# Performance work log

Hardware: AMD Instinct MI355X
Metric: run time of the kernel (lower is better)

Reference implementation:

```python
import jax, jax.numpy as jnp
import numpy as np

DIM = 256; DIM_HEAD = 32; HEADS = DIM // DIM_HEAD; WSZ = 8; D4 = DIM // 4
EPS = 1e-5
SCALE = DIM_HEAD ** -0.5


def _rel_pos_indices(wsz):
    pos = np.arange(wsz)
    grid = np.stack(np.meshgrid(pos, pos, indexing='ij')).reshape(2, -1).T  # (w*w, 2)
    rel = grid[:, None] - grid[None, :] + wsz - 1
    return jnp.asarray((rel * np.array([2 * wsz - 1, 1])).sum(-1))  # (w*w, w*w)


def _ln(x, g, b):
    m = x.mean(-1, keepdims=True)
    v = jnp.var(x, axis=-1, keepdims=True)
    return (x - m) / jnp.sqrt(v + EPS) * g + b


def setup_inputs() -> dict:
    key = jax.random.key(0)
    ks = jax.random.split(key, 8)
    inner = HEADS * DIM_HEAD
    def n(k, shape, s=0.02):
        return jax.random.normal(k, shape, dtype=jnp.float32) * s
    return {
        "x": jax.random.normal(ks[0], (2, DIM, 256, 256), dtype=jnp.float32),
        "norm_g": jnp.ones((1, DIM, 1, 1), jnp.float32),
        "norm_b": jnp.zeros((1, DIM, 1, 1), jnp.float32),
        "w_qkv": n(ks[1], (3 * inner, DIM)),
        "w_out": n(ks[2], (DIM, inner)),
        "b_out": jnp.zeros((DIM,), jnp.float32),
        "dpb_w1": n(ks[3], (D4, 2), 0.5), "dpb_b1": jnp.zeros((D4,), jnp.float32),
        "dpb_g1": jnp.ones((D4,), jnp.float32), "dpb_beta1": jnp.zeros((D4,), jnp.float32),
        "dpb_w2": n(ks[4], (D4, D4), 0.1), "dpb_b2": jnp.zeros((D4,), jnp.float32),
        "dpb_g2": jnp.ones((D4,), jnp.float32), "dpb_beta2": jnp.zeros((D4,), jnp.float32),
        "dpb_w3": n(ks[5], (D4, D4), 0.1), "dpb_b3": jnp.zeros((D4,), jnp.float32),
        "dpb_g3": jnp.ones((D4,), jnp.float32), "dpb_beta3": jnp.zeros((D4,), jnp.float32),
        "dpb_w4": n(ks[6], (1, D4), 0.1), "dpb_b4": jnp.zeros((1,), jnp.float32),
    }


def reference(x, norm_g, norm_b, w_qkv, w_out, b_out,
              dpb_w1, dpb_b1, dpb_g1, dpb_beta1,
              dpb_w2, dpb_b2, dpb_g2, dpb_beta2,
              dpb_w3, dpb_b3, dpb_g3, dpb_beta3,
              dpb_w4, dpb_b4):
    B, D, H, W = x.shape
    nh, nw = H // WSZ, W // WSZ
    # channel-first LayerNorm (stats over dim=1, biased variance)
    mean = x.mean(axis=1, keepdims=True)
    var = jnp.var(x, axis=1, keepdims=True)
    xn = (x - mean) / jnp.sqrt(var + EPS) * norm_g + norm_b
    # 'short' windowing: b d (h s1) (w s2) -> (b h w) d (s1 s2)
    xw = xn.reshape(B, D, nh, WSZ, nw, WSZ).transpose(0, 2, 4, 1, 3, 5)
    xw = xw.reshape(B * nh * nw, D, WSZ * WSZ)
    # 1x1 conv QKV == matmul over channel dim
    qkv = jnp.einsum('ed,bdn->ben', w_qkv, xw)
    q, k, v = jnp.split(qkv, 3, axis=1)
    to_heads = lambda t: t.reshape(-1, HEADS, DIM_HEAD, WSZ * WSZ).transpose(0, 1, 3, 2)
    q, k, v = to_heads(q) * SCALE, to_heads(k), to_heads(v)
    sim = jnp.einsum('bhid,bhjd->bhij', q, k)  # [Bw, H, 64, 64]
    # dynamic position bias MLP over relative coordinates in [-wsz, wsz]
    pos = jnp.arange(-WSZ, WSZ + 1, dtype=x.dtype)
    rel = jnp.stack(jnp.meshgrid(pos, pos, indexing='ij')).reshape(2, -1).T  # ((2w+1)^2, 2)
    h1 = jax.nn.relu(_ln(rel @ dpb_w1.T + dpb_b1, dpb_g1, dpb_beta1))
    h2 = jax.nn.relu(_ln(h1 @ dpb_w2.T + dpb_b2, dpb_g2, dpb_beta2))
    h3 = jax.nn.relu(_ln(h2 @ dpb_w3.T + dpb_b3, dpb_g3, dpb_beta3))
    biases = (h3 @ dpb_w4.T + dpb_b4)[:, 0]
    sim = sim + biases[_rel_pos_indices(WSZ)]
    attn = jax.nn.softmax(sim, axis=-1)
    out = jnp.einsum('bhij,bhjd->bhid', attn, v)
    # b h (x y) d -> b (h d) (x y)
    out = out.transpose(0, 1, 3, 2).reshape(-1, HEADS * DIM_HEAD, WSZ * WSZ)
    out = jnp.einsum('de,ben->bdn', w_out, out) + b_out[None, :, None]
    # (b h w) d s1 s2 -> b d (h s1) (w s2)
    out = out.reshape(B, nh, nw, D, WSZ, WSZ).transpose(0, 3, 1, 4, 2, 5).reshape(B, D, H, W)
    return out
```

## Files before the change

kernel.cpp:

```cpp
#include <hip/hip_runtime.h>


typedef __attribute__((ext_vector_type(8))) short bf16x8;
typedef __attribute__((ext_vector_type(4))) short bf16x4;
typedef __attribute__((ext_vector_type(4))) float f32x4;

#define LOG2E    1.44269504088896f
#define QK_SCALE 0.17677669529663687f

__device__ __forceinline__ short f2b(float f) {
  union { float f; unsigned u; } v; v.f = f;
  unsigned r = v.u + 0x7FFFu + ((v.u >> 16) & 1u);
  return (short)(r >> 16);
}

__device__ __forceinline__ unsigned pk2(float a, float b) {
  union { float f; unsigned u; } ua, ub; ua.f = a; ub.f = b;
#if __has_builtin(__builtin_amdgcn_perm)
  return __builtin_amdgcn_perm(ub.u + 0x8000u, ua.u + 0x8000u, 0x07060302u);
#else
  return ((ua.u + 0x8000u) >> 16) | ((ub.u + 0x8000u) & 0xFFFF0000u);
#endif
}

__device__ __forceinline__ bf16x8 mk8(unsigned a, unsigned b, unsigned c, unsigned d) {
  union { unsigned u[4]; bf16x8 v; } x; x.u[0] = a; x.u[1] = b; x.u[2] = c; x.u[3] = d;
  return x.v;
}
__device__ __forceinline__ bf16x4 mk4(unsigned a, unsigned b) {
  union { unsigned u[2]; bf16x4 v; } x; x.u[0] = a; x.u[1] = b; return x.v;
}

__device__ __forceinline__ f32x4 mfma16(bf16x4 a, bf16x4 b, f32x4 c) {
#if __has_builtin(__builtin_amdgcn_mfma_f32_16x16x16bf16_1k)
  return __builtin_amdgcn_mfma_f32_16x16x16bf16_1k(a, b, c, 0, 0, 0);
#else
  f32x4 d;
  asm volatile("v_mfma_f32_16x16x16_bf16 %0, %1, %2, %3"
               : "=&v"(d) : "v"(a), "v"(b), "v"(c));
  return d;
#endif
}

__global__ __launch_bounds__(256)
void wconv_kernel(const float* __restrict__ wqkv, const float* __restrict__ wout,
                  short* __restrict__ wq_t, short* __restrict__ wo_t) {
  int t = (blockIdx.x * 256 + threadIdx.x) * 8;
  if (t < 196608) {
    int blk = t >> 9, l = (t & 511) >> 3;
    int et = blk >> 3, kt = blk & 7;
    int e = et * 16 + (l & 15);
    int d = kt * 32 + (l >> 4) * 8;
    const float* src = wqkv + e * 256 + d;
    float sc = (e < 256) ? QK_SCALE * LOG2E : 1.0f;
    bf16x8 pk;
    #pragma unroll
    for (int el = 0; el < 8; ++el) pk[el] = f2b(src[el] * sc);
    *(bf16x8*)(wq_t + t) = pk;
  } else if (t < 262144) {
    int o = t - 196608;
    int blk = o >> 9, l = (o & 511) >> 3;
    int dt = blk >> 3, kt = blk & 7;
    int dout = dt * 16 + (l & 15);
    int e = kt * 32 + (l >> 4) * 8;
    const float* src = wout + dout * 256 + e;
    bf16x8 pk;
    #pragma unroll
    for (int el = 0; el < 8; ++el) pk[el] = f2b(src[el]);
    *(bf16x8*)(wo_t + o) = pk;
  }
}

__device__ __forceinline__ float wave_sum64(float v) {
  v += __shfl_xor(v, 1);  v += __shfl_xor(v, 2);  v += __shfl_xor(v, 4);
  v += __shfl_xor(v, 8);  v += __shfl_xor(v, 16); v += __shfl_xor(v, 32);
  return v;
}

__global__ __launch_bounds__(64)
void dpb_kernel(const float* __restrict__ w1, const float* __restrict__ b1,
                const float* __restrict__ g1, const float* __restrict__ be1,
                const float* __restrict__ w2, const float* __restrict__ b2,
                const float* __restrict__ g2, const float* __restrict__ be2,
                const float* __restrict__ w3, const float* __restrict__ b3,
                const float* __restrict__ g3, const float* __restrict__ be3,
                const float* __restrict__ w4, const float* __restrict__ b4,
                float* __restrict__ sb) {
  __shared__ float h[64];
  __shared__ float wbuf[4096];
  const int f = threadIdx.x;
  const int pos = blockIdx.x;
  const float py = (float)(pos / 17) - 8.0f;
  const float px = (float)(pos % 17) - 8.0f;

  float a = py * w1[2 * f] + px * w1[2 * f + 1] + b1[f];
  {
    float m = wave_sum64(a) * (1.f / 64.f);
    float d = a - m;
    float var = wave_sum64(d * d) * (1.f / 64.f);
    a = fmaxf(d * rsqrtf(var + 1e-5f) * g1[f] + be1[f], 0.f);
  }
  h[f] = a;
  __threadfence_block();

  #pragma unroll 8
  for (int k = 0; k < 64; ++k) wbuf[k * 64 + f] = w2[k * 64 + f];
  __threadfence_block();
  float acc = b2[f];
  #pragma unroll 8
  for (int k = 0; k < 64; ++k) {
    int g = (k + f) & 63;
    acc += wbuf[f * 64 + g] * h[g];
  }
  {
    float m = wave_sum64(acc) * (1.f / 64.f);
    float d = acc - m;
    float var = wave_sum64(d * d) * (1.f / 64.f);
    acc = fmaxf(d * rsqrtf(var + 1e-5f) * g2[f] + be2[f], 0.f);
  }
  __threadfence_block();
  h[f] = acc;
  __threadfence_block();

  #pragma unroll 8
  for (int k = 0; k < 64; ++k) wbuf[k * 64 + f] = w3[k * 64 + f];
  __threadfence_block();
  float acc3 = b3[f];
  #pragma unroll 8
  for (int k = 0; k < 64; ++k) {
    int g = (k + f) & 63;
    acc3 += wbuf[f * 64 + g] * h[g];
  }
  {
    float m = wave_sum64(acc3) * (1.f / 64.f);
    float d = acc3 - m;
    float var = wave_sum64(d * d) * (1.f / 64.f);
    acc3 = fmaxf(d * rsqrtf(var + 1e-5f) * g3[f] + be3[f], 0.f);
  }
  float o = wave_sum64(w4[f] * acc3);
  if (f == 0) sb[pos] = o + b4[0];
}

__global__ __launch_bounds__(512)
void expand_kernel(const float* __restrict__ sb, float* __restrict__ tblf) {
  int idx = blockIdx.x * 512 + threadIdx.x;
  int it = idx >> 10, jt = (idx >> 8) & 3, ln = (idx >> 2) & 63, jj = idx & 3;
  int rr = ln & 15, gg = ln >> 4;
  int i = it * 16 + rr;
  int j = jt * 16 + gg * 4 + jj;
  int dy = (i >> 3) - (j >> 3) + 7;
  int dx = (i & 7) - (j & 7) + 7;
  tblf[idx] = sb[dy * 15 + dx] * LOG2E;
}

#define SM_XA   0
#define SM_PS   65536
#define SM_SIZE 73728
#define XASWZ(p) ((((p) & 7) << 4) ^ ((((p) >> 3) & 3) << 7))

__global__ __launch_bounds__(512)
void attn_kernel(const float* __restrict__ x, const float* __restrict__ gnorm,
                 const float* __restrict__ bnorm, const short* __restrict__ wq_t,
                 const short* __restrict__ wo_t, const float* __restrict__ bout,
                 const float* __restrict__ tblf, float* __restrict__ out) {
  __shared__ __align__(16) char smem[SM_SIZE];
  const int t = threadIdx.x;
  const int lane = t & 63;
  const int w = t >> 6;
  const int r = lane & 15;
  const int gq = lane >> 4;

  const int bid = blockIdx.x;
  const int b   = bid >> 9;
  const int wh  = (bid >> 4) & 31;
  const int ww2 = bid & 15;
  const int R = wh * 8, C = ww2 * 16;

  const int n = lane;
  const int d0 = w * 32;
  float* PS = (float*)(smem + SM_PS);
  float xv[2][32];
  #pragma unroll
  for (int h = 0; h < 2; ++h) {
    const float* xb = x + (((size_t)(b * 256 + d0)) << 16) +
                      (R + 4 * h + (n >> 4)) * 256 + C + (n & 15);
    float s1 = 0.f, s2v = 0.f;
    #pragma unroll
    for (int i = 0; i < 32; ++i) {
      float v = xb[(size_t)i << 16];
      xv[h][i] = v; s1 += v; s2v += v * v;
    }
    PS[h * 1024 + w * 64 + n] = s1;
    PS[h * 1024 + 512 + w * 64 + n] = s2v;
  }
  __syncthreads();
  #pragma unroll
  for (int h = 0; h < 2; ++h) {
    float a = 0.f, q2 = 0.f;
    #pragma unroll
    for (int dg = 0; dg < 8; ++dg) {
      a  += PS[h * 1024 + dg * 64 + n];
      q2 += PS[h * 1024 + 512 + dg * 64 + n];
    }
    float mean = a * (1.f / 256.f);
    float var = q2 * (1.f / 256.f) - mean * mean;
    float rstd = rsqrtf(var + 1e-5f);
    int p2 = (4 * h + (n >> 4)) * 16 + (n & 15);
    #pragma unroll
    for (int c = 0; c < 4; ++c) {
      float xn[8];
      #pragma unroll
      for (int e = 0; e < 8; ++e) {
        int d = d0 + c * 8 + e;
        xn[e] = (xv[h][c * 8 + e] - mean) * rstd * gnorm[d] + bnorm[d];
      }
      *(bf16x8*)(smem + SM_XA + (p2 << 9) + ((((d0 + c * 8) << 1)) ^ XASWZ(p2))) =
          mk8(pk2(xn[0], xn[1]), pk2(xn[2], xn[3]), pk2(xn[4], xn[5]), pk2(xn[6], xn[7]));
    }
  }
  __syncthreads();

  const f32x4 vzero = {0.f, 0.f, 0.f, 0.f};

  #define QKV_SWAP(PP, ACC)                                                     \
    {                                                                           \
      _Pragma("unroll")                                                         \
      for (int nt = 0; nt < 2; ++nt)                                            \
        _Pragma("unroll")                                                       \
        for (int t4 = 0; t4 < 4; ++t4) ACC[nt][t4] = vzero;                     \
      _Pragma("unroll")                                                         \
      for (int kt = 0; kt < 8; ++kt) {                                          \
        bf16x8 bfr0 = *(const bf16x8*)(wq_t + (((((PP) * 16 + w * 2 + 0) * 8 + kt) << 9) + lane * 8)); \
        bf16x8 bfr1 = *(const bf16x8*)(wq_t + (((((PP) * 16 + w * 2 + 1) * 8 + kt) << 9) + lane * 8)); \
        bf16x8 afr[4];                                                          \
        _Pragma("unroll")                                                       \
        for (int t4 = 0; t4 < 4; ++t4) {                                        \
          int p2 = (t4 * 2 + (r >> 3)) * 16 + wl * 8 + (r & 7);                 \
          afr[t4] = *(const bf16x8*)(smem + SM_XA + (p2 << 9) + ((((kt * 32 + gq * 8) << 1)) ^ XASWZ(p2))); \
        }                                                                       \
        _Pragma("unroll")                                                       \
        for (int t4 = 0; t4 < 4; ++t4) {                                        \
          ACC[0][t4] = __builtin_amdgcn_mfma_f32_16x16x32_bf16(bfr0, afr[t4], ACC[0][t4], 0, 0, 0); \
          ACC[1][t4] = __builtin_amdgcn_mfma_f32_16x16x32_bf16(bfr1, afr[t4], ACC[1][t4], 0, 0, 0); \
        }                                                                       \
      }                                                                         \
    }

  f32x4 o2[2][2][4];
  #pragma unroll
  for (int wl = 0; wl < 2; ++wl) {
    bf16x4 kpk[2][4], qpk[2][4];
    {
      f32x4 acc[2][4];
      QKV_SWAP(1, acc);
      #pragma unroll
      for (int kb = 0; kb < 2; ++kb)
        #pragma unroll
        for (int jt = 0; jt < 4; ++jt)
          kpk[kb][jt] = mk4(pk2(acc[kb][jt][0], acc[kb][jt][1]),
                            pk2(acc[kb][jt][2], acc[kb][jt][3]));
    }
    {
      f32x4 acc[2][4];
      QKV_SWAP(0, acc);
      #pragma unroll
      for (int kb = 0; kb < 2; ++kb)
        #pragma unroll
        for (int it = 0; it < 4; ++it)
          qpk[kb][it] = mk4(pk2(acc[kb][it][0], acc[kb][it][1]),
                            pk2(acc[kb][it][2], acc[kb][it][3]));
    }
    bf16x4 va8[4][2];
    {
      f32x4 vacc[4][2];
      #pragma unroll
      for (int mt = 0; mt < 4; ++mt)
        #pragma unroll
        for (int nt = 0; nt < 2; ++nt) vacc[mt][nt] = vzero;
      #pragma unroll
      for (int kt = 0; kt < 8; ++kt) {
        bf16x8 bfr0 = *(const bf16x8*)(wq_t + ((((2 * 16 + w * 2 + 0) * 8 + kt) << 9) + lane * 8));
        bf16x8 bfr1 = *(const bf16x8*)(wq_t + ((((2 * 16 + w * 2 + 1) * 8 + kt) << 9) + lane * 8));
        bf16x8 afr[4];
        #pragma unroll
        for (int mt = 0; mt < 4; ++mt) {
          int p2 = (mt * 2 + (r >> 3)) * 16 + wl * 8 + (r & 7);
          afr[mt] = *(const bf16x8*)(smem + SM_XA + (p2 << 9) + ((((kt * 32 + gq * 8) << 1)) ^ XASWZ(p2)));
        }
        #pragma unroll
        for (int mt = 0; mt < 4; ++mt) {
          vacc[mt][0] = __builtin_amdgcn_mfma_f32_16x16x32_bf16(afr[mt], bfr0, vacc[mt][0], 0, 0, 0);
          vacc[mt][1] = __builtin_amdgcn_mfma_f32_16x16x32_bf16(afr[mt], bfr1, vacc[mt][1], 0, 0, 0);
        }
      }
      #pragma unroll
      for (int mt = 0; mt < 4; ++mt)
        #pragma unroll
        for (int nt = 0; nt < 2; ++nt)
          va8[mt][nt] = mk4(pk2(vacc[mt][nt][0], vacc[mt][nt][1]),
                            pk2(vacc[mt][nt][2], vacc[mt][nt][3]));
    }

    #pragma unroll
    for (int nt = 0; nt < 2; ++nt)
      #pragma unroll
      for (int it = 0; it < 4; ++it) o2[wl][nt][it] = vzero;
    __builtin_amdgcn_s_setprio(1);
    #pragma unroll
    for (int it = 0; it < 4; ++it) {
      f32x4 sc[4];
      #pragma unroll
      for (int jt = 0; jt < 4; ++jt) {
        sc[jt] = mfma16(kpk[0][jt], qpk[0][it], vzero);
        sc[jt] = mfma16(kpk[1][jt], qpk[1][it], sc[jt]);
      }
      float m0 = -1e30f;
      #pragma unroll
      for (int jt = 0; jt < 4; ++jt) {
        f32x4 bj = *(const f32x4*)(tblf + (((it * 4 + jt) * 64 + lane) << 2));
        #pragma unroll
        for (int jj = 0; jj < 4; ++jj) {
          sc[jt][jj] += bj[jj];
          m0 = fmaxf(m0, sc[jt][jj]);
        }
      }
      m0 = fmaxf(m0, __shfl_xor(m0, 16));
      m0 = fmaxf(m0, __shfl_xor(m0, 32));
      float sum = 0.f;
      #pragma unroll
      for (int jt = 0; jt < 4; ++jt)
        #pragma unroll
        for (int jj = 0; jj < 4; ++jj) {
          float e = exp2f(sc[jt][jj] - m0);
          sc[jt][jj] = e; sum += e;
        }
      sum += __shfl_xor(sum, 16);
      sum += __shfl_xor(sum, 32);
      float pinv = 1.0f / sum;
      bf16x4 ppk[4];
      #pragma unroll
      for (int jt = 0; jt < 4; ++jt)
        ppk[jt] = mk4(pk2(sc[jt][0] * pinv, sc[jt][1] * pinv),
                      pk2(sc[jt][2] * pinv, sc[jt][3] * pinv));
      #pragma unroll
      for (int mt = 0; mt < 4; ++mt)
        #pragma unroll
        for (int nt = 0; nt < 2; ++nt)
          o2[wl][nt][it] = mfma16(va8[mt][nt], ppk[mt], o2[wl][nt][it]);
    }
    __builtin_amdgcn_s_setprio(0);
  }
  __syncthreads();

  #pragma unroll
  for (int wl = 0; wl < 2; ++wl)
    #pragma unroll
    for (int nt = 0; nt < 2; ++nt)
      #pragma unroll
      for (int it = 0; it < 4; ++it) {
        int pw = it * 16 + r;
        int p2 = ((pw >> 3) << 4) + (wl << 3) + (pw & 7);
        int e = (w << 5) + (nt << 4) + (gq << 2);
        *(bf16x4*)(smem + SM_XA + (p2 << 9) + (((e << 1)) ^ XASWZ(p2))) =
            mk4(pk2(o2[wl][nt][it][0], o2[wl][nt][it][1]),
                pk2(o2[wl][nt][it][2], o2[wl][nt][it][3]));
      }
  __syncthreads();

  float bov[2];
  bov[0] = bout[w * 32 + r];
  bov[1] = bout[w * 32 + 16 + r];

  #pragma unroll
  for (int ck = 0; ck < 2; ++ck) {
    f32x4 c3[4][2];
    #pragma unroll
    for (int mt = 0; mt < 4; ++mt)
      #pragma unroll
      for (int nt = 0; nt < 2; ++nt) c3[mt][nt] = vzero;
    __builtin_amdgcn_s_setprio(1);
    #pragma unroll
    for (int kt = 0; kt < 8; ++kt) {
      bf16x8 woB[2];
      #pragma unroll
      for (int nt = 0; nt < 2; ++nt)
        woB[nt] = *(const bf16x8*)(wo_t + ((((w * 2 + nt) * 8 + kt) << 9) + lane * 8));
      bf16x8 af[4];
      #pragma unroll
      for (int mt = 0; mt < 4; ++mt) {
        int p2 = ck * 64 + mt * 16 + r;
        af[mt] = *(const bf16x8*)(smem + SM_XA + (p2 << 9) + ((((kt * 32 + gq * 8) << 1)) ^ XASWZ(p2)));
      }
      #pragma unroll
      for (int mt = 0; mt < 4; ++mt)
        #pragma unroll
        for (int nt = 0; nt < 2; ++nt)
          c3[mt][nt] = __builtin_amdgcn_mfma_f32_16x16x32_bf16(af[mt], woB[nt], c3[mt][nt], 0, 0, 0);
    }
    __builtin_amdgcn_s_setprio(0);
    #pragma unroll
    for (int mt = 0; mt < 4; ++mt)
      #pragma unroll
      for (int nt = 0; nt < 2; ++nt) {
        int dout = w * 32 + nt * 16 + r;
        int row = ck * 4 + mt;
        f32x4 v = c3[mt][nt];
        v[0] += bov[nt]; v[1] += bov[nt]; v[2] += bov[nt]; v[3] += bov[nt];
        *(f32x4*)(out + (((size_t)(b * 256 + dout)) << 16) + (R + row) * 256 + C + gq * 4) = v;
      }
  }
  #undef QKV_SWAP
}

extern "C" void kernel_launch(void* const* d_in, const int* in_sizes, int n_in,
                              void* d_out, int out_size, void* d_ws, size_t ws_size,
                              hipStream_t stream) {
  const float* x     = (const float*)d_in[0];
  const float* gnorm = (const float*)d_in[1];
  const float* bnorm = (const float*)d_in[2];
  const float* wqkv  = (const float*)d_in[3];
  const float* wout  = (const float*)d_in[4];
  const float* bout  = (const float*)d_in[5];
  const float* w1  = (const float*)d_in[6];
  const float* b1  = (const float*)d_in[7];
  const float* g1  = (const float*)d_in[8];
  const float* be1 = (const float*)d_in[9];
  const float* w2  = (const float*)d_in[10];
  const float* b2  = (const float*)d_in[11];
  const float* g2  = (const float*)d_in[12];
  const float* be2 = (const float*)d_in[13];
  const float* w3  = (const float*)d_in[14];
  const float* b3  = (const float*)d_in[15];
  const float* g3  = (const float*)d_in[16];
  const float* be3 = (const float*)d_in[17];
  const float* w4  = (const float*)d_in[18];
  const float* b4  = (const float*)d_in[19];

  short* wq_t = (short*)d_ws;
  short* wo_t = wq_t + 196608;
  float* sb   = (float*)((char*)d_ws + 524288);
  float* tblf = (float*)((char*)d_ws + 528384);

  wconv_kernel<<<dim3(128), dim3(256), 0, stream>>>(wqkv, wout, wq_t, wo_t);
  dpb_kernel<<<dim3(289), dim3(64), 0, stream>>>(
      w1, b1, g1, be1, w2, b2, g2, be2, w3, b3, g3, be3, w4, b4, sb);
  expand_kernel<<<dim3(8), dim3(512), 0, stream>>>(sb, tblf);

  attn_kernel<<<dim3(1024), dim3(512), 0, stream>>>(
      x, gnorm, bnorm, wq_t, wo_t, bout, tblf, (float*)d_out);
}
```

Baseline: 193.5 us.

## Merge prep kernels, fuse Q/K projection, defer softmax normalization, hoist Wout loads

Combines the weight-conversion and position-bias MLP kernels into one launch, which removes a kernel launch. Computes Q and K in a single MFMA loop that shares the A-fragment loads. Drops the softmax max-subtraction and applies the 1/sum scaling to the attention output rather than to the probabilities. Preloads all Wout fragments into registers before the output projection. Skipping max-subtraction risks exp2 overflow if scores are large, and the extra registers may lower occupancy.

Result: faster. 177.7 us (-8.1%).

```diff
diff --git a/kernel.cpp b/kernel.cpp
--- a/kernel.cpp
+++ b/kernel.cpp
@@ -42,54 +42,57 @@
 #endif
 }
 
-__global__ __launch_bounds__(256)
-void wconv_kernel(const float* __restrict__ wqkv, const float* __restrict__ wout,
-                  short* __restrict__ wq_t, short* __restrict__ wo_t) {
-  int t = (blockIdx.x * 256 + threadIdx.x) * 8;
-  if (t < 196608) {
-    int blk = t >> 9, l = (t & 511) >> 3;
-    int et = blk >> 3, kt = blk & 7;
-    int e = et * 16 + (l & 15);
-    int d = kt * 32 + (l >> 4) * 8;
-    const float* src = wqkv + e * 256 + d;
-    float sc = (e < 256) ? QK_SCALE * LOG2E : 1.0f;
-    bf16x8 pk;
-    #pragma unroll
-    for (int el = 0; el < 8; ++el) pk[el] = f2b(src[el] * sc);
-    *(bf16x8*)(wq_t + t) = pk;
-  } else if (t < 262144) {
-    int o = t - 196608;
-    int blk = o >> 9, l = (o & 511) >> 3;
-    int dt = blk >> 3, kt = blk & 7;
-    int dout = dt * 16 + (l & 15);
-    int e = kt * 32 + (l >> 4) * 8;
-    const float* src = wout + dout * 256 + e;
-    bf16x8 pk;
-    #pragma unroll
-    for (int el = 0; el < 8; ++el) pk[el] = f2b(src[el]);
-    *(bf16x8*)(wo_t + o) = pk;
-  }
-}
-
 __device__ __forceinline__ float wave_sum64(float v) {
   v += __shfl_xor(v, 1);  v += __shfl_xor(v, 2);  v += __shfl_xor(v, 4);
   v += __shfl_xor(v, 8);  v += __shfl_xor(v, 16); v += __shfl_xor(v, 32);
   return v;
 }
 
-__global__ __launch_bounds__(64)
-void dpb_kernel(const float* __restrict__ w1, const float* __restrict__ b1,
-                const float* __restrict__ g1, const float* __restrict__ be1,
-                const float* __restrict__ w2, const float* __restrict__ b2,
-                const float* __restrict__ g2, const float* __restrict__ be2,
-                const float* __restrict__ w3, const float* __restrict__ b3,
-                const float* __restrict__ g3, const float* __restrict__ be3,
-                const float* __restrict__ w4, const float* __restrict__ b4,
-                float* __restrict__ sb) {
+__global__ __launch_bounds__(256)
+void prep_kernel(const float* __restrict__ wqkv, const float* __restrict__ wout,
+                 const float* __restrict__ w1, const float* __restrict__ b1,
+                 const float* __restrict__ g1, const float* __restrict__ be1,
+                 const float* __restrict__ w2, const float* __restrict__ b2,
+                 const float* __restrict__ g2, const float* __restrict__ be2,
+                 const float* __restrict__ w3, const float* __restrict__ b3,
+                 const float* __restrict__ g3, const float* __restrict__ be3,
+                 const float* __restrict__ w4, const float* __restrict__ b4,
+                 short* __restrict__ wq_t, short* __restrict__ wo_t,
+                 float* __restrict__ sb) {
   __shared__ float h[64];
   __shared__ float wbuf[4096];
+
+  if (blockIdx.x < 128) {
+    int t = (blockIdx.x * 256 + threadIdx.x) * 8;
+    if (t < 196608) {
+      int blk = t >> 9, l = (t & 511) >> 3;
+      int et = blk >> 3, kt = blk & 7;
+      int e = et * 16 + (l & 15);
+      int d = kt * 32 + (l >> 4) * 8;
+      const float* src = wqkv + e * 256 + d;
+      float sc = (e < 256) ? QK_SCALE * LOG2E : 1.0f;
+      bf16x8 pk;
+      #pragma unroll
+      for (int el = 0; el < 8; ++el) pk[el] = f2b(src[el] * sc);
+      *(bf16x8*)(wq_t + t) = pk;
+    } else {
+      int o = t - 196608;
+      int blk = o >> 9, l = (o & 511) >> 3;
+      int dt = blk >> 3, kt = blk & 7;
+      int dout = dt * 16 + (l & 15);
+      int e = kt * 32 + (l >> 4) * 8;
+      const float* src = wout + dout * 256 + e;
+      bf16x8 pk;
+      #pragma unroll
+      for (int el = 0; el < 8; ++el) pk[el] = f2b(src[el]);
+      *(bf16x8*)(wo_t + o) = pk;
+    }
+    return;
+  }
+
+  if (threadIdx.x >= 64) return;
   const int f = threadIdx.x;
-  const int pos = blockIdx.x;
+  const int pos = blockIdx.x - 128;
   const float py = (float)(pos / 17) - 8.0f;
   const float px = (float)(pos % 17) - 8.0f;
 
@@ -222,53 +225,46 @@
 
   const f32x4 vzero = {0.f, 0.f, 0.f, 0.f};
 
-  #define QKV_SWAP(PP, ACC)                                                     \
-    {                                                                           \
-      _Pragma("unroll")                                                         \
-      for (int nt = 0; nt < 2; ++nt)                                            \
-        _Pragma("unroll")                                                       \
-        for (int t4 = 0; t4 < 4; ++t4) ACC[nt][t4] = vzero;                     \
-      _Pragma("unroll")                                                         \
-      for (int kt = 0; kt < 8; ++kt) {                                          \
-        bf16x8 bfr0 = *(const bf16x8*)(wq_t + (((((PP) * 16 + w * 2 + 0) * 8 + kt) << 9) + lane * 8)); \
-        bf16x8 bfr1 = *(const bf16x8*)(wq_t + (((((PP) * 16 + w * 2 + 1) * 8 + kt) << 9) + lane * 8)); \
-        bf16x8 afr[4];                                                          \
-        _Pragma("unroll")                                                       \
-        for (int t4 = 0; t4 < 4; ++t4) {                                        \
-          int p2 = (t4 * 2 + (r >> 3)) * 16 + wl * 8 + (r & 7);                 \
-          afr[t4] = *(const bf16x8*)(smem + SM_XA + (p2 << 9) + ((((kt * 32 + gq * 8) << 1)) ^ XASWZ(p2))); \
-        }                                                                       \
-        _Pragma("unroll")                                                       \
-        for (int t4 = 0; t4 < 4; ++t4) {                                        \
-          ACC[0][t4] = __builtin_amdgcn_mfma_f32_16x16x32_bf16(bfr0, afr[t4], ACC[0][t4], 0, 0, 0); \
-          ACC[1][t4] = __builtin_amdgcn_mfma_f32_16x16x32_bf16(bfr1, afr[t4], ACC[1][t4], 0, 0, 0); \
-        }                                                                       \
-      }                                                                         \
-    }
-
   f32x4 o2[2][2][4];
+  float pinv[2][4];
   #pragma unroll
   for (int wl = 0; wl < 2; ++wl) {
     bf16x4 kpk[2][4], qpk[2][4];
     {
-      f32x4 acc[2][4];
-      QKV_SWAP(1, acc);
+      f32x4 aq[2][4], ak[2][4];
+      #pragma unroll
+      for (int nt = 0; nt < 2; ++nt)
+        #pragma unroll
+        for (int t4 = 0; t4 < 4; ++t4) { aq[nt][t4] = vzero; ak[nt][t4] = vzero; }
+      #pragma unroll
+      for (int kt = 0; kt < 8; ++kt) {
+        bf16x8 bq0 = *(const bf16x8*)(wq_t + ((((0 * 16 + w * 2 + 0) * 8 + kt) << 9) + lane * 8));
+        bf16x8 bq1 = *(const bf16x8*)(wq_t + ((((0 * 16 + w * 2 + 1) * 8 + kt) << 9) + lane * 8));
+        bf16x8 bk0 = *(const bf16x8*)(wq_t + ((((1 * 16 + w * 2 + 0) * 8 + kt) << 9) + lane * 8));
+        bf16x8 bk1 = *(const bf16x8*)(wq_t + ((((1 * 16 + w * 2 + 1) * 8 + kt) << 9) + lane * 8));
+        bf16x8 afr[4];
+        #pragma unroll
+        for (int t4 = 0; t4 < 4; ++t4) {
+          int p2 = (t4 * 2 + (r >> 3)) * 16 + wl * 8 + (r & 7);
+          afr[t4] = *(const bf16x8*)(smem + SM_XA + (p2 << 9) + ((((kt * 32 + gq * 8) << 1)) ^ XASWZ(p2)));
+        }
+        #pragma unroll
+        for (int t4 = 0; t4 < 4; ++t4) {
+          aq[0][t4] = __builtin_amdgcn_mfma_f32_16x16x32_bf16(bq0, afr[t4], aq[0][t4], 0, 0, 0);
+          aq[1][t4] = __builtin_amdgcn_mfma_f32_16x16x32_bf16(bq1, afr[t4], aq[1][t4], 0, 0, 0);
+          ak[0][t4] = __builtin_amdgcn_mfma_f32_16x16x32_bf16(bk0, afr[t4], ak[0][t4], 0, 0, 0);
+          ak[1][t4] = __builtin_amdgcn_mfma_f32_16x16x32_bf16(bk1, afr[t4], ak[1][t4], 0, 0, 0);
+        }
+      }
       #pragma unroll
       for (int kb = 0; kb < 2; ++kb)
         #pragma unroll
-        for (int jt = 0; jt < 4; ++jt)
-          kpk[kb][jt] = mk4(pk2(acc[kb][jt][0], acc[kb][jt][1]),
-                            pk2(acc[kb][jt][2], acc[kb][jt][3]));
-    }
-    {
-      f32x4 acc[2][4];
-      QKV_SWAP(0, acc);
-      #pragma unroll
-      for (int kb = 0; kb < 2; ++kb)
-        #pragma unroll
-        for (int it = 0; it < 4; ++it)
-          qpk[kb][it] = mk4(pk2(acc[kb][it][0], acc[kb][it][1]),
-                            pk2(acc[kb][it][2], acc[kb][it][3]));
+        for (int t4 = 0; t4 < 4; ++t4) {
+          qpk[kb][t4] = mk4(pk2(aq[kb][t4][0], aq[kb][t4][1]),
+                            pk2(aq[kb][t4][2], aq[kb][t4][3]));
+          kpk[kb][t4] = mk4(pk2(ak[kb][t4][0], ak[kb][t4][1]),
+                            pk2(ak[kb][t4][2], ak[kb][t4][3]));
+        }
     }
     bf16x4 va8[4][2];
     {
@@ -314,34 +310,23 @@
         sc[jt] = mfma16(kpk[0][jt], qpk[0][it], vzero);
         sc[jt] = mfma16(kpk[1][jt], qpk[1][it], sc[jt]);
       }
-      float m0 = -1e30f;
+      float sum = 0.f;
       #pragma unroll
       for (int jt = 0; jt < 4; ++jt) {
         f32x4 bj = *(const f32x4*)(tblf + (((it * 4 + jt) * 64 + lane) << 2));
         #pragma unroll
         for (int jj = 0; jj < 4; ++jj) {
-          sc[jt][jj] += bj[jj];
-          m0 = fmaxf(m0, sc[jt][jj]);
-        }
-      }
-      m0 = fmaxf(m0, __shfl_xor(m0, 16));
-      m0 = fmaxf(m0, __shfl_xor(m0, 32));
-      float sum = 0.f;
-      #pragma unroll
-      for (int jt = 0; jt < 4; ++jt)
-        #pragma unroll
-        for (int jj = 0; jj < 4; ++jj) {
-          float e = exp2f(sc[jt][jj] - m0);
+          float e = exp2f(sc[jt][jj] + bj[jj]);
           sc[jt][jj] = e; sum += e;
         }
+      }
       sum += __shfl_xor(sum, 16);
       sum += __shfl_xor(sum, 32);
-      float pinv = 1.0f / sum;
+      pinv[wl][it] = 1.0f / sum;
       bf16x4 ppk[4];
       #pragma unroll
       for (int jt = 0; jt < 4; ++jt)
-        ppk[jt] = mk4(pk2(sc[jt][0] * pinv, sc[jt][1] * pinv),
-                      pk2(sc[jt][2] * pinv, sc[jt][3] * pinv));
+        ppk[jt] = mk4(pk2(sc[jt][0], sc[jt][1]), pk2(sc[jt][2], sc[jt][3]));
       #pragma unroll
       for (int mt = 0; mt < 4; ++mt)
         #pragma unroll
@@ -358,20 +343,27 @@
     for (int nt = 0; nt < 2; ++nt)
       #pragma unroll
       for (int it = 0; it < 4; ++it) {
+        float pv = pinv[wl][it];
         int pw = it * 16 + r;
         int p2 = ((pw >> 3) << 4) + (wl << 3) + (pw & 7);
         int e = (w << 5) + (nt << 4) + (gq << 2);
         *(bf16x4*)(smem + SM_XA + (p2 << 9) + (((e << 1)) ^ XASWZ(p2))) =
-            mk4(pk2(o2[wl][nt][it][0], o2[wl][nt][it][1]),
-                pk2(o2[wl][nt][it][2], o2[wl][nt][it][3]));
+            mk4(pk2(o2[wl][nt][it][0] * pv, o2[wl][nt][it][1] * pv),
+                pk2(o2[wl][nt][it][2] * pv, o2[wl][nt][it][3] * pv));
       }
   __syncthreads();
 
   float bov[2];
   bov[0] = bout[w * 32 + r];
   bov[1] = bout[w * 32 + 16 + r];
-
+  bf16x8 woB[2][8];
   #pragma unroll
+  for (int nt = 0; nt < 2; ++nt)
+    #pragma unroll
+    for (int kt = 0; kt < 8; ++kt)
+      woB[nt][kt] = *(const bf16x8*)(wo_t + ((((w * 2 + nt) * 8 + kt) << 9) + lane * 8));
+
+  #pragma unroll 1
   for (int ck = 0; ck < 2; ++ck) {
     f32x4 c3[4][2];
     #pragma unroll
@@ -381,10 +373,6 @@
     __builtin_amdgcn_s_setprio(1);
     #pragma unroll
     for (int kt = 0; kt < 8; ++kt) {
-      bf16x8 woB[2];
-      #pragma unroll
-      for (int nt = 0; nt < 2; ++nt)
-        woB[nt] = *(const bf16x8*)(wo_t + ((((w * 2 + nt) * 8 + kt) << 9) + lane * 8));
       bf16x8 af[4];
       #pragma unroll
       for (int mt = 0; mt < 4; ++mt) {
@@ -395,7 +383,7 @@
       for (int mt = 0; mt < 4; ++mt)
         #pragma unroll
         for (int nt = 0; nt < 2; ++nt)
-          c3[mt][nt] = __builtin_amdgcn_mfma_f32_16x16x32_bf16(af[mt], woB[nt], c3[mt][nt], 0, 0, 0);
+          c3[mt][nt] = __builtin_amdgcn_mfma_f32_16x16x32_bf16(af[mt], woB[nt][kt], c3[mt][nt], 0, 0, 0);
     }
     __builtin_amdgcn_s_setprio(0);
     #pragma unroll
@@ -409,7 +397,6 @@
         *(f32x4*)(out + (((size_t)(b * 256 + dout)) << 16) + (R + row) * 256 + C + gq * 4) = v;
       }
   }
-  #undef QKV_SWAP
 }
 
 extern "C" void kernel_launch(void* const* d_in, const int* in_sizes, int n_in,
@@ -441,9 +428,9 @@
   float* sb   = (float*)((char*)d_ws + 524288);
   float* tblf = (float*)((char*)d_ws + 528384);
 
-  wconv_kernel<<<dim3(128), dim3(256), 0, stream>>>(wqkv, wout, wq_t, wo_t);
-  dpb_kernel<<<dim3(289), dim3(64), 0, stream>>>(
-      w1, b1, g1, be1, w2, b2, g2, be2, w3, b3, g3, be3, w4, b4, sb);
+  prep_kernel<<<dim3(417), dim3(256), 0, stream>>>(
+      wqkv, wout, w1, b1, g1, be1, w2, b2, g2, be2, w3, b3, g3, be3, w4, b4,
+      wq_t, wo_t, sb);
   expand_kernel<<<dim3(8), dim3(512), 0, stream>>>(sb, tblf);
 
   attn_kernel<<<dim3(1024), dim3(512), 0, stream>>>(
```
